# Optimization experiments

Measured on AMD Instinct MI355X. Metric: run time of the kernel, lower is better.

The kernel has to match this reference:

```python
import jax, jax.numpy as jnp
import numpy as np

XLIM = 10.0
N_BINS = 200
LATTICE = 12.42
N_O, N_H = 64, 128
T, R = 1000, 8


def setup_inputs() -> dict:
    key = jax.random.key(0)
    k1, k2 = jax.random.split(key)
    n = N_O + N_H
    stacked_radii = jax.random.uniform(k1, (T, R, n, 3), dtype=jnp.float32) * LATTICE
    lattices = jnp.full((3,), LATTICE, dtype=jnp.float32)
    gt_rdf = jax.random.uniform(k2, (3, N_BINS), dtype=jnp.float32)
    idx_O = jnp.arange(N_O, dtype=jnp.int32)
    idx_H = jnp.arange(N_H, dtype=jnp.int32) + N_O
    return {"stacked_radii": stacked_radii, "lattices": lattices,
            "gt_rdf": gt_rdf, "idx_O": idx_O, "idx_H": idx_H}


def reference(stacked_radii, lattices, gt_rdf, idx_O, idx_H):
    bins = jnp.linspace(1e-6, XLIM, N_BINS + 1, dtype=jnp.float32)
    # np.histogram normalization: rho * (4/3)pi (r_hi^3 - r_lo^3)
    shell = (4.0 / 3.0) * np.pi * (bins[1:] ** 3 - bins[:-1] ** 3)
    vol = jnp.prod(lattices)
    # wrap positions into the box (data_seq / L % 1 * L)
    x = stacked_radii / lattices % 1.0 * lattices
    x = jnp.transpose(x, (1, 0, 2, 3))  # [R, T, N, 3]

    def pair_rdf(x_rep, i0, i1):
        x0 = x_rep[:, i0]  # [T, n0, 3]
        x1 = x_rep[:, i1]  # [T, n1, 3]
        # all-pairs minimum-image distance under PBC
        delta = jnp.abs(x0[:, :, None, :] - x1[:, None, :, :])  # [T, n0, n1, 3]
        delta = jnp.where(delta > 0.5 * lattices, delta - lattices, delta)
        d = jnp.sqrt(jnp.sum(delta ** 2, axis=-1)).ravel()
        n_pairs = d.shape[0]  # includes zeros, matches original rho
        mask = (d != 0.0) & (d >= bins[0]) & (d <= bins[-1])
        bidx = jnp.clip(jnp.searchsorted(bins, d, side='right') - 1, 0, N_BINS - 1)
        hist = jax.ops.segment_sum(mask.astype(jnp.float32), bidx, num_segments=N_BINS)
        rho = n_pairs / vol
        return hist / (rho * shell)  # [N_BINS]

    pairs = [(idx_O, idx_O), (idx_H, idx_H), (idx_H, idx_O)]  # OO, HH, HO
    # sequential over replicas (like the original python loop) to bound memory
    rdfs = [jax.lax.map(lambda xr, i0=i0, i1=i1: pair_rdf(xr, i0, i1), x)
            for (i0, i1) in pairs]  # each [R, N_BINS]
    maes = jnp.stack([XLIM * jnp.mean(jnp.abs(r - g), axis=-1)
                      for r, g in zip(rdfs, gt_rdf)], axis=0)  # [3, R]
    max_maes = jnp.max(maes, axis=0)  # [R]
    rdf_stack = jnp.concatenate(rdfs, axis=-1)  # [R, 3*N_BINS]
    return rdf_stack, max_maes
```

## Files before the change

kernel.cpp:

```cpp
#include <hip/hip_runtime.h>
#include <math.h>

#define NUM_T   1000
#define NUM_R   8
#define NBINS   200
#define FPB     2
#define TTSZ    224
#define TYSTR   217
#define NCOL    4
#define HWORDS  (3*TYSTR*NCOL)

__device__ __forceinline__ float approx_sqrt(float x) {
    float r; asm("v_sqrt_f32 %0, %1" : "=v"(r) : "v"(x)); return r;
}
__device__ __forceinline__ float fract_(float x) {
#if __has_builtin(__builtin_amdgcn_fractf)
    return __builtin_amdgcn_fractf(x);
#else
    return x - floorf(x);
#endif
}

__global__ __launch_bounds__(256, 8) void rdf_hist_kernel(
    const float* __restrict__ radii,
    const float* __restrict__ lat,
    unsigned int* __restrict__ gh)
{
    #pragma clang fp contract(off)
    __shared__ float4 posOx[96], posH0[96], posH1[96];
    __shared__ float TT[TTSZ];
    __shared__ __align__(16) unsigned int hist[HWORDS];

    const int tid = threadIdx.x;

    if (tid < TTSZ) {
        float v;
        if (tid <= 200) {
            float b;
            if (tid < NBINS) {
                const double step = (10.0 - 1e-6) / 200.0;
                b = (float)(1e-6 + (double)tid * step);
            } else {
                b = __uint_as_float(__float_as_uint(10.0f) + 1u);
            }
            unsigned lo = 0u, hi = 0x7F800000u;
            while (lo < hi) {
                unsigned mid = (lo + hi) >> 1;
                if (sqrtf(__uint_as_float(mid)) >= b) hi = mid; else lo = mid + 1;
            }
            v = __uint_as_float(lo);
        } else {
            v = __uint_as_float(0x7F800000u);
        }
        TT[tid] = v;
    }
    for (int i = tid; i < HWORDS; i += 256) hist[i] = 0u;

    const float Lx = lat[0], Ly = lat[1], Lz = lat[2];
    __syncthreads();

    const int col = tid & (NCOL - 1);

#define PAIRV(PI, PJ, TB, W)                                                 \
    {                                                                        \
        float tx = (PI).x - (PJ).x;                                          \
        float ty = (PI).y - (PJ).y;                                          \
        float tz = (PI).z - (PJ).z;                                          \
        float ax = fminf(fabsf(tx), Lx - fabsf(tx));                         \
        float ay = fminf(fabsf(ty), Ly - fabsf(ty));                         \
        float az = fminf(fabsf(tz), Lz - fabsf(tz));                         \
        float s  = (ax*ax + ay*ay) + az*az;                                  \
        float z  = approx_sqrt(s * 400.0f);                                  \
        int   k  = (int)z;                                                   \
        float m  = fract_(z);                                                \
        bool amb = fabsf(m - 0.5f) > 0.49980f;                               \
        if (__builtin_expect(__any(amb), 0)) {                               \
            float tlo = TT[k], thi = TT[k + 1];                              \
            k += ((s >= thi) ? 1 : 0) - ((s < tlo) ? 1 : 0);                 \
            if (k < 0) k = 216;                                              \
        }                                                                    \
        atomicAdd(&hist[(TB) + (k << 2)], (W));                              \
    }

    const int rep   = blockIdx.x & (NUM_R - 1);
    const int chunk = blockIdx.x / NUM_R;
    const int l     = tid & 63;
    const int q     = tid >> 6;
    const int tbOO  = col;
    const int tbHH  = col + (TYSTR << 2);
    const int tbHO  = col + (2 * TYSTR << 2);

    float rvx = 0.f, rvy = 0.f, rvz = 0.f;
    {
        const float* s0 = radii + ((size_t)(chunk * FPB) * NUM_R + rep) * (192 * 3);
        if (tid < 192) { rvx = s0[tid*3+0]; rvy = s0[tid*3+1]; rvz = s0[tid*3+2]; }
    }

    #pragma unroll 1
    for (int f = 0; f < FPB; ++f) {
        __syncthreads();
        if (tid < 192) {
            float ux = rvx / Lx; ux -= floorf(ux);
            float uy = rvy / Ly; uy -= floorf(uy);
            float uz = rvz / Lz; uz -= floorf(uz);
            float4 p = make_float4(ux*Lx, uy*Ly, uz*Lz, 0.0f);
            if (tid < 64)       { posOx[tid] = p;  if (tid < 32) posOx[tid+64] = p; }
            else if (tid < 128) { int h = tid-64;  posH0[h] = p; if (h < 32) posH0[h+64] = p; }
            else                { int h = tid-128; posH1[h] = p; if (h < 32) posH1[h+64] = p; }
        }
        __syncthreads();

        if (f + 1 < FPB && tid < 192) {
            const float* s1 = radii + ((size_t)(chunk * FPB + f + 1) * NUM_R + rep) * (192 * 3);
            rvx = s1[tid*3+0]; rvy = s1[tid*3+1]; rvz = s1[tid*3+2];
        }

        const float4 piO = posOx[l];
        const float4 pi0 = posH0[l];
        const float4 pi1 = posH1[l];
        const int jb = l + q + 1;

        {
            float4 pjs[8];
            #pragma unroll
            for (int it = 0; it < 8; ++it) pjs[it] = posOx[jb + 4*it];
            #pragma unroll
            for (int it = 0; it < 7; ++it) PAIRV(piO, pjs[it], tbOO, 2u)
            if (q < 3 || l < 32) PAIRV(piO, pjs[7], tbOO, 2u)
        }
        {
            float4 pjs[8];
            #pragma unroll
            for (int it = 0; it < 8; ++it) pjs[it] = posH0[jb + 4*it];
            #pragma unroll
            for (int it = 0; it < 7; ++it) PAIRV(pi0, pjs[it], tbHH, 2u)
            if (q < 3 || l < 32) PAIRV(pi0, pjs[7], tbHH, 2u)
        }
        {
            float4 pjs[8];
            #pragma unroll
            for (int it = 0; it < 8; ++it) pjs[it] = posH1[jb + 4*it];
            #pragma unroll
            for (int it = 0; it < 7; ++it) PAIRV(pi1, pjs[it], tbHH, 2u)
            if (q < 3 || l < 32) PAIRV(pi1, pjs[7], tbHH, 2u)
        }
        #pragma unroll 1
        for (int b2 = 0; b2 < 2; ++b2) {
            float4 pjc[8];
            #pragma unroll
            for (int jj = 0; jj < 8; ++jj) pjc[jj] = posH1[q*16 + b2*8 + jj];
            #pragma unroll
            for (int jj = 0; jj < 8; ++jj) PAIRV(pi0, pjc[jj], tbHH, 2u)
        }
        #pragma unroll 1
        for (int b2 = 0; b2 < 2; ++b2) {
            float4 pjc[8];
            #pragma unroll
            for (int jj = 0; jj < 8; ++jj) pjc[jj] = posOx[q*16 + b2*8 + jj];
            #pragma unroll
            for (int jj = 0; jj < 8; ++jj) {
                PAIRV(pi0, pjc[jj], tbHO, 1u)
                PAIRV(pi1, pjc[jj], tbHO, 1u)
            }
        }
    }
#undef PAIRV

    __syncthreads();
    for (int idx = tid; idx < 3 * NBINS; idx += 256) {
        const int p = idx / 200;
        const int b = idx - p * 200;
        const uint4 v = *reinterpret_cast<const uint4*>(&hist[(p * TYSTR + b) << 2]);
        unsigned sum = (v.x + v.y) + (v.z + v.w);
        if (sum) atomicAdd(&gh[rep * 3 * NBINS + idx], sum);
    }
}

__global__ __launch_bounds__(256) void rdf_final_kernel(
    const unsigned int* __restrict__ gh,
    const float* __restrict__ gt,
    const float* __restrict__ lat,
    float* __restrict__ out)
{
    #pragma clang fp contract(off)
    const int rep = blockIdx.x;
    const int tid = threadIdx.x;
    __shared__ float bins[NBINS + 1];
    __shared__ float red[256];

    for (int i = tid; i <= NBINS; i += 256) {
        const double step = (10.0 - 1e-6) / 200.0;
        bins[i] = (i == NBINS) ? 10.0f : (float)(1e-6 + (double)i * step);
    }
    __syncthreads();

    const float vol = (lat[0] * lat[1]) * lat[2];
    const float C   = 4.18879020478639053f;
    const int npairs[3] = { NUM_T*64*64, NUM_T*128*128, NUM_T*128*64 };

    float maxmae = -3.0e38f;
    for (int p = 0; p < 3; ++p) {
        float diff = 0.0f;
        if (tid < NBINS) {
            float b0 = bins[tid], b1 = bins[tid + 1];
            float shell = C * (b1*b1*b1 - b0*b0*b0);
            float rho = (float)npairs[p] / vol;
            float g = (float)gh[(rep*3 + p)*NBINS + tid] / (rho * shell);
            out[rep*3*NBINS + p*NBINS + tid] = g;
            diff = fabsf(g - gt[p*NBINS + tid]);
        }
        red[tid] = diff;
        __syncthreads();
        for (int s = 128; s > 0; s >>= 1) {
            if (tid < s) red[tid] += red[tid + s];
            __syncthreads();
        }
        if (tid == 0) {
            float mae = 10.0f * (red[0] / 200.0f);
            if (mae > maxmae) maxmae = mae;
        }
        __syncthreads();
    }
    if (tid == 0) out[NUM_R*3*NBINS + rep] = maxmae;
}

extern "C" void kernel_launch(void* const* d_in, const int* in_sizes, int n_in,
                              void* d_out, int out_size, void* d_ws, size_t ws_size,
                              hipStream_t stream) {
    const float* radii = (const float*)d_in[0];
    const float* lat   = (const float*)d_in[1];
    const float* gt    = (const float*)d_in[2];
    unsigned int* gh   = (unsigned int*)d_ws;

    hipMemsetAsync(gh, 0, NUM_R * 3 * NBINS * sizeof(unsigned int), stream);

    dim3 grid(NUM_R * (NUM_T / FPB));
    hipLaunchKernelGGL(rdf_hist_kernel, grid, dim3(256), 0, stream,
                       radii, lat, gh);
    hipLaunchKernelGGL(rdf_final_kernel, dim3(NUM_R), dim3(256), 0, stream,
                       gh, gt, lat, (float*)d_out);
}
```

Before: 93.57 us.

## Pair two i-atoms per lane and rotate section order across wavefronts

```diff
diff --git a/kernel.cpp b/kernel.cpp
--- a/kernel.cpp
+++ b/kernel.cpp
@@ -82,6 +82,18 @@
         atomicAdd(&hist[(TB) + (k << 2)], (W));                              \
     }
 
+#define ROTSEC(ARR, PIA, PIB, TB)                                            \
+    {                                                                        \
+        float4 pja[4];                                                       \
+        _Pragma("unroll")                                                    \
+        for (int it = 0; it < 4; ++it) pja[it] = ARR[jb2 + 8*it];            \
+        _Pragma("unroll")                                                    \
+        for (int it = 0; it < 4; ++it) {                                     \
+            PAIRV(PIB, pja[it], TB, 2u)                                      \
+            if (it < 3 || q < 3 || l < 32) PAIRV(PIA, pja[it], TB, 2u)       \
+        }                                                                    \
+    }
+
     const int rep   = blockIdx.x & (NUM_R - 1);
     const int chunk = blockIdx.x / NUM_R;
     const int l     = tid & 63;
@@ -115,55 +127,53 @@
             rvx = s1[tid*3+0]; rvy = s1[tid*3+1]; rvz = s1[tid*3+2];
         }
 
-        const float4 piO = posOx[l];
-        const float4 pi0 = posH0[l];
-        const float4 pi1 = posH1[l];
-        const int jb = l + q + 1;
-
-        {
-            float4 pjs[8];
-            #pragma unroll
-            for (int it = 0; it < 8; ++it) pjs[it] = posOx[jb + 4*it];
-            #pragma unroll
-            for (int it = 0; it < 7; ++it) PAIRV(piO, pjs[it], tbOO, 2u)
-            if (q < 3 || l < 32) PAIRV(piO, pjs[7], tbOO, 2u)
-        }
-        {
-            float4 pjs[8];
-            #pragma unroll
-            for (int it = 0; it < 8; ++it) pjs[it] = posH0[jb + 4*it];
-            #pragma unroll
-            for (int it = 0; it < 7; ++it) PAIRV(pi0, pjs[it], tbHH, 2u)
-            if (q < 3 || l < 32) PAIRV(pi0, pjs[7], tbHH, 2u)
-        }
-        {
-            float4 pjs[8];
-            #pragma unroll
-            for (int it = 0; it < 8; ++it) pjs[it] = posH1[jb + 4*it];
-            #pragma unroll
-            for (int it = 0; it < 7; ++it) PAIRV(pi1, pjs[it], tbHH, 2u)
-            if (q < 3 || l < 32) PAIRV(pi1, pjs[7], tbHH, 2u)
-        }
-        #pragma unroll 1
-        for (int b2 = 0; b2 < 2; ++b2) {
-            float4 pjc[8];
-            #pragma unroll
-            for (int jj = 0; jj < 8; ++jj) pjc[jj] = posH1[q*16 + b2*8 + jj];
-            #pragma unroll
-            for (int jj = 0; jj < 8; ++jj) PAIRV(pi0, pjc[jj], tbHH, 2u)
-        }
-        #pragma unroll 1
-        for (int b2 = 0; b2 < 2; ++b2) {
-            float4 pjc[8];
-            #pragma unroll
-            for (int jj = 0; jj < 8; ++jj) pjc[jj] = posOx[q*16 + b2*8 + jj];
-            #pragma unroll
-            for (int jj = 0; jj < 8; ++jj) {
-                PAIRV(pi0, pjc[jj], tbHO, 1u)
-                PAIRV(pi1, pjc[jj], tbHO, 1u)
+        const float4 piO  = posOx[l];
+        const float4 piOb = posOx[l + 1];
+        const float4 pi0  = posH0[l];
+        const float4 pi0b = posH0[l + 1];
+        const float4 pi1  = posH1[l];
+        const float4 pi1b = posH1[l + 1];
+        const int jb2 = l + 2*q + 2;
+
+        #pragma unroll
+        for (int sid = 0; sid < 5; ++sid) {
+            switch ((sid + q) % 5) {
+            case 0:
+                ROTSEC(posOx, piO, piOb, tbOO)
+                break;
+            case 1:
+                ROTSEC(posH0, pi0, pi0b, tbHH)
+                break;
+            case 2:
+                ROTSEC(posH1, pi1, pi1b, tbHH)
+                break;
+            case 3:
+                #pragma unroll 1
+                for (int b2 = 0; b2 < 2; ++b2) {
+                    float4 pjc[8];
+                    #pragma unroll
+                    for (int jj = 0; jj < 8; ++jj) pjc[jj] = posH1[q*16 + b2*8 + jj];
+                    #pragma unroll
+                    for (int jj = 0; jj < 8; ++jj) PAIRV(pi0, pjc[jj], tbHH, 2u)
+                }
+                break;
+            default:
+                #pragma unroll 1
+                for (int b2 = 0; b2 < 2; ++b2) {
+                    float4 pjc[8];
+                    #pragma unroll
+                    for (int jj = 0; jj < 8; ++jj) pjc[jj] = posOx[q*16 + b2*8 + jj];
+                    #pragma unroll
+                    for (int jj = 0; jj < 8; ++jj) {
+                        PAIRV(pi0, pjc[jj], tbHO, 1u)
+                        PAIRV(pi1, pjc[jj], tbHO, 1u)
+                    }
+                }
+                break;
             }
         }
     }
+#undef ROTSEC
 #undef PAIRV
 
     __syncthreads();
```

Result: slower. 99.37 us (+6.2%).
